# Optimization experiments

Measured on AMD Instinct MI355X. Metric: run time of the kernel, lower is better.

Reference implementation:

```python
import jax, jax.numpy as jnp
import numpy as np

EPS = 1e-5
DEPTH = 3
NQ = 12


def _bn(x, g, b):
    # BatchNorm1d in training mode: batch statistics, biased variance
    mu = x.mean(0)
    var = x.var(0)
    return (x - mu) / jnp.sqrt(var + EPS) * g + b


def _ln(x, g, b):
    mu = x.mean(-1, keepdims=True)
    var = x.var(-1, keepdims=True)
    return (x - mu) / jnp.sqrt(var + EPS) * g + b


def _apply_1q(s, U, q):
    # s: [B, 2^NQ] complex; U: [2,2] (shared) or [B,2,2] (per-sample); qubit q = q-th MSB
    B = s.shape[0]
    s = s.reshape(B, 2 ** q, 2, -1)
    sub = 'ij,bajc->baic' if U.ndim == 2 else 'bij,bajc->baic'
    return jnp.einsum(sub, U, s).reshape(B, -1)


def _apply_cry(s, theta, c):
    # controlled-Ry(theta): control qubit c, target qubit c+1 (adjacent)
    B = s.shape[0]
    s = s.reshape(B, 2 ** c, 2, 2, -1)
    co = jnp.cos(theta / 2).astype(s.dtype)
    si = jnp.sin(theta / 2).astype(s.dtype)
    s1 = s[:, :, 1]  # control = |1> block
    new1 = jnp.stack([co * s1[:, :, 0] - si * s1[:, :, 1],
                      si * s1[:, :, 0] + co * s1[:, :, 1]], axis=2)
    s = jnp.concatenate([s[:, :, :1], new1[:, :, None]], axis=2)
    return s.reshape(B, -1)


def _measure(s):
    # P(qubit q measures |1>) for each qubit
    p = jnp.abs(s) ** 2  # [B, 2^NQ]
    B = p.shape[0]
    probs = [p.reshape(B, 2 ** q, 2, -1).sum(axis=(1, 3))[:, 1] for q in range(NQ)]
    return jnp.stack(probs, axis=1)  # [B, NQ]


def _rot_mats(rot):
    # fused Rz(rz) @ Ry(ry) @ Rx(rx) for each (depth, qubit) -> [DEPTH, NQ, 2, 2]
    hx, hy, hz = rot[..., 0] / 2, rot[..., 1] / 2, rot[..., 2] / 2
    cx, sx = jnp.cos(hx), jnp.sin(hx)
    Rx = jnp.stack([jnp.stack([cx + 0j, -1j * sx], -1),
                    jnp.stack([-1j * sx, cx + 0j], -1)], -2)
    cy, sy = jnp.cos(hy), jnp.sin(hy)
    Ry = jnp.stack([jnp.stack([cy, -sy], -1),
                    jnp.stack([sy, cy], -1)], -2).astype(jnp.complex64)
    ez = jnp.exp(-1j * hz)
    z0 = jnp.zeros_like(ez)
    Rz = jnp.stack([jnp.stack([ez, z0], -1),
                    jnp.stack([z0, jnp.conj(ez)], -1)], -2)
    return jnp.einsum('...ij,...jk,...kl->...il', Rz, Ry, Rx).astype(jnp.complex64)


def _quantum_layer(x, We, be, gi, bi, rot, ent, Wd, bd, go, bo):
    e = jnp.tanh(_bn(x @ We.T + be, gi, bi))  # [B, NQ]
    nrm = jnp.linalg.norm(e, axis=1, keepdims=True)
    a = jnp.where(nrm > 0, e / nrm, e)        # per-sample L2-normalized amplitudes
    B = x.shape[0]
    s = jnp.zeros((B, 2 ** NQ), jnp.complex64).at[:, 0].set(1.0)
    # amplitude encoding: Ry(2*arcsin(|a|)) then phase pi (sign) if a<0 -> diag(1,-1)@Ry
    ang = 2.0 * jnp.arcsin(jnp.clip(jnp.abs(a), 0.0, 1.0))
    c, si = jnp.cos(ang / 2), jnp.sin(ang / 2)
    sg = jnp.where(a < 0, -1.0, 1.0)
    for q in range(NQ):
        U = jnp.stack([jnp.stack([c[:, q], -si[:, q]], -1),
                       jnp.stack([sg[:, q] * si[:, q], sg[:, q] * c[:, q]], -1)],
                      -2).astype(jnp.complex64)  # [B,2,2]
        s = _apply_1q(s, U, q)
    # parameterized circuit: per-qubit fused Rz.Ry.Rx, then nearest-neighbor CRy chain
    U = _rot_mats(rot)
    for d in range(DEPTH):
        for q in range(NQ):
            s = _apply_1q(s, U[d, q], q)
        for i in range(NQ - 1):
            s = _apply_cry(s, ent[d, i], i)
    m = _measure(s)
    return _bn(m @ Wd.T + bd, go, bo)


def setup_inputs() -> dict:
    key = jax.random.key(0)
    ks = jax.random.split(key, 16)
    B, IN, H1, H2, H3, OUT = 512, 512, 512, 512, 1024, 256

    def lin(k, o, i):
        k1, k2 = jax.random.split(k)
        lim = 1.0 / np.sqrt(i)
        return (jax.random.uniform(k1, (o, i), jnp.float32, -lim, lim),
                jax.random.uniform(k2, (o,), jnp.float32, -lim, lim))

    qWe0, qbe0 = lin(ks[1], NQ, IN)
    qWd0, qbd0 = lin(ks[2], H1, NQ)
    qWe1, qbe1 = lin(ks[3], NQ, H1)
    qWd1, qbd1 = lin(ks[4], H2, NQ)
    W2, b2 = lin(ks[5], H3, H2)
    Wo, bo = lin(ks[6], OUT, H3)
    return {
        'x': jax.random.normal(ks[0], (B, IN), jnp.float32),
        'qWe0': qWe0, 'qbe0': qbe0,
        'qgi0': jnp.ones(NQ), 'qbi0': jnp.zeros(NQ),
        'rot0': 0.1 * jax.random.normal(ks[7], (DEPTH, NQ, 3), jnp.float32),
        'ent0': 0.1 * jax.random.normal(ks[8], (DEPTH, NQ - 1), jnp.float32),
        'qWd0': qWd0, 'qbd0': qbd0,
        'qgo0': jnp.ones(H1), 'qbo0': jnp.zeros(H1),
        'qWe1': qWe1, 'qbe1': qbe1,
        'qgi1': jnp.ones(NQ), 'qbi1': jnp.zeros(NQ),
        'rot1': 0.1 * jax.random.normal(ks[9], (DEPTH, NQ, 3), jnp.float32),
        'ent1': 0.1 * jax.random.normal(ks[10], (DEPTH, NQ - 1), jnp.float32),
        'qWd1': qWd1, 'qbd1': qbd1,
        'qgo1': jnp.ones(H2), 'qbo1': jnp.zeros(H2),
        'W2': W2, 'b2': b2, 'ln2g': jnp.ones(H3), 'ln2b': jnp.zeros(H3),
        'Wo': Wo, 'bo': bo, 'lnog': jnp.ones(OUT), 'lnob': jnp.zeros(OUT),
    }


def reference(x, qWe0, qbe0, qgi0, qbi0, rot0, ent0, qWd0, qbd0, qgo0, qbo0,
              qWe1, qbe1, qgi1, qbi1, rot1, ent1, qWd1, qbd1, qgo1, qbo1,
              W2, b2, ln2g, ln2b, Wo, bo, lnog, lnob):
    h = _quantum_layer(x, qWe0, qbe0, qgi0, qbi0, rot0, ent0, qWd0, qbd0, qgo0, qbo0)
    h = _quantum_layer(h, qWe1, qbe1, qgi1, qbi1, rot1, ent1, qWd1, qbd1, qgo1, qbo1)
    h = jax.nn.relu(_ln(h @ W2.T + b2, ln2g, ln2b))  # classical block (dropout = identity, eval)
    return _ln(h @ Wo.T + bo, lnog, lnob)
```

## Files before the change

### kernel.cpp

```cpp
#include <hip/hip_runtime.h>
#include <math.h>

#define EPS   1e-5f
#define NQ    12
#define DEPTH 3
#define BATCH 512
#define DIM   4096

__device__ inline float2 cmul(float2 a, float2 b) {
    return make_float2(a.x*b.x - a.y*b.y, a.x*b.y + a.y*b.x);
}
__device__ inline float2 cmac2(float2 ua, float2 s, float2 ub, float2 p) {
    return make_float2(ua.x*s.x - ua.y*s.y + ub.x*p.x - ub.y*p.y,
                       ua.x*s.y + ua.y*s.x + ub.x*p.y + ub.y*p.x);
}

__global__ void consts_kernel(const float* __restrict__ rot0, const float* __restrict__ ent0,
                              const float* __restrict__ rot1, const float* __restrict__ ent1,
                              float2* __restrict__ Uc, float2* __restrict__ Cc) {
    int t = threadIdx.x;
    if (t < 72) {
        int layer = t / 36, rem = t % 36, d = rem / 12, q = rem % 12;
        const float* rot = layer ? rot1 : rot0;
        float hx = 0.5f * rot[(d*NQ + q)*3 + 0];
        float hy = 0.5f * rot[(d*NQ + q)*3 + 1];
        float hz = 0.5f * rot[(d*NQ + q)*3 + 2];
        float cx = cosf(hx), sx = sinf(hx);
        float cy = cosf(hy), sy = sinf(hy);
        float2 m00 = make_float2( cy*cx,  sy*sx);
        float2 m01 = make_float2(-sy*cx, -cy*sx);
        float2 m10 = make_float2( sy*cx, -cy*sx);
        float2 m11 = make_float2( cy*cx, -sy*sx);
        float2 ez  = make_float2(cosf(hz), -sinf(hz));
        float2 ezc = make_float2(ez.x, -ez.y);
        float2* U = Uc + t*4;
        U[0] = cmul(ez,  m00);
        U[1] = cmul(ez,  m01);
        U[2] = cmul(ezc, m10);
        U[3] = cmul(ezc, m11);
    } else if (t < 72 + 66) {
        int idx = t - 72, layer = idx / 33, rem = idx % 33;
        const float* ent = layer ? ent1 : ent0;
        float th = 0.5f * ent[rem];
        Cc[idx] = make_float2(cosf(th), sinf(th));
    }
}

__global__ __launch_bounds__(256) void encode_rm_kernel(
        const float* __restrict__ X, const float* __restrict__ We,
        const float* __restrict__ be, float* __restrict__ Yraw) {
    __shared__ float w[NQ][512];
    int tid = threadIdx.x;
    {
        const float4* src = (const float4*)We;
        float4* dst = (float4*)&w[0][0];
        #pragma unroll
        for (int i = tid; i < NQ*512/4; i += 256) dst[i] = src[i];
    }
    __syncthreads();
    int wave = tid >> 6, lane = tid & 63;
    int b = blockIdx.x * 4 + wave;
    const float4* xr = (const float4*)(X + (size_t)b * 512);
    float acc[NQ] = {};
    #pragma unroll
    for (int j = 0; j < 2; ++j) {
        float4 xv = xr[lane + 64*j];
        #pragma unroll
        for (int q = 0; q < NQ; ++q) {
            float4 wv = ((const float4*)&w[q][0])[lane + 64*j];
            acc[q] += xv.x*wv.x + xv.y*wv.y + xv.z*wv.z + xv.w*wv.w;
        }
    }
    #pragma unroll
    for (int q = 0; q < NQ; ++q) {
        float v = acc[q];
        #pragma unroll
        for (int off = 32; off; off >>= 1) v += __shfl_xor(v, off);
        if (lane == q) Yraw[b*NQ + q] = v + be[q];
    }
}

__global__ __launch_bounds__(512) void bn_tanh_kernel(
        const float* __restrict__ Yraw,
        const float* __restrict__ gi, const float* __restrict__ bi,
        float* __restrict__ A) {
    int b = threadIdx.x;
    float v[NQ];
    #pragma unroll
    for (int q = 0; q < NQ; ++q) v[q] = Yraw[b*NQ + q];
    __shared__ float2 red[NQ][8];
    int lane = b & 63, wave = b >> 6;
    #pragma unroll
    for (int q = 0; q < NQ; ++q) {
        float2 t = make_float2(v[q], v[q]*v[q]);
        for (int off = 32; off; off >>= 1) { t.x += __shfl_down(t.x, off); t.y += __shfl_down(t.y, off); }
        if (lane == 0) red[q][wave] = t;
    }
    __syncthreads();
    #pragma unroll
    for (int q = 0; q < NQ; ++q) {
        float s = 0.f, s2 = 0.f;
        #pragma unroll
        for (int wv = 0; wv < 8; ++wv) { s += red[q][wv].x; s2 += red[q][wv].y; }
        float mu  = s  * (1.f/512.f);
        float var = s2 * (1.f/512.f) - mu*mu;
        A[b*NQ + q] = tanhf((v[q] - mu) * rsqrtf(var + EPS) * gi[q] + bi[q]);
    }
}

__device__ inline int swz(int a) { return a ^ ((a >> 4) & 15); }

template<int L> __device__ inline int ampl(int tid, int k) {
    if constexpr (L == 1) return (k << 8) | tid;
    else if constexpr (L == 2) return ((tid & 0xE0) << 4) | (k << 5) | (tid & 0x1F);
    else if constexpr (L == 3) return ((tid & 0xFC) << 4) | (k << 2) | (tid & 3);
    else return (tid << 4) | k;
}

template<int F, int T>
__device__ inline void remap(float2* amp, float2* lds2, int tid) {
    #pragma unroll
    for (int k = 0; k < 16; ++k) lds2[swz(ampl<F>(tid, k))] = amp[k];
    __syncthreads();
    #pragma unroll
    for (int k = 0; k < 16; ++k) amp[k] = lds2[swz(ampl<T>(tid, k))];
    __syncthreads();
}

template<int BP>
__device__ inline void one_q(float2* amp, float2 u00, float2 u01, float2 u10, float2 u11) {
    #pragma unroll
    for (int g = 0; g < 8; ++g) {
        const int j0 = ((g >> BP) << (BP+1)) | (g & ((1<<BP)-1));
        const int j1 = j0 | (1 << BP);
        float2 a0 = amp[j0], a1 = amp[j1];
        amp[j0] = cmac2(u00, a0, u01, a1);
        amp[j1] = cmac2(u10, a0, u11, a1);
    }
}

template<int CB, int TB>
__device__ inline void cry_rr(float2* amp, float co, float si) {
    #pragma unroll
    for (int m = 0; m < 16; ++m) {
        if (((m >> CB) & 1) && !((m >> TB) & 1)) {
            const int j1 = m | (1 << TB);
            float2 a0 = amp[m], a1 = amp[j1];
            amp[m]  = make_float2(co*a0.x - si*a1.x, co*a0.y - si*a1.y);
            amp[j1] = make_float2(si*a0.x + co*a1.x, si*a0.y + co*a1.y);
        }
    }
}

__global__ __launch_bounds__(256) void qsim_kernel(
        const float* __restrict__ A, const float2* __restrict__ UcAll,
        const float2* __restrict__ CcAll, int layer, float* __restrict__ mout) {
    int b = blockIdx.x, tid = threadIdx.x;
    const float2* Uc = UcAll + layer * DEPTH * NQ * 4;
    const float2* Cc = CcAll + layer * DEPTH * (NQ - 1);
    __shared__ float2 lds2[DIM];
    __shared__ float red[NQ][4];

    float av[NQ]; float n2 = 0.f;
    #pragma unroll
    for (int q = 0; q < NQ; ++q) { av[q] = A[b*NQ + q]; n2 += av[q]*av[q]; }
    float scn = (n2 > 0.f) ? rsqrtf(n2) : 1.f;
    float2 v0[NQ], v1[NQ];
    #pragma unroll
    for (int q = 0; q < NQ; ++q) {
        float a  = av[q] * scn;
        float sv = fminf(fabsf(a), 1.f);
        float c  = sqrtf(fmaxf(1.f - sv*sv, 0.f));
        float ss = (a < 0.f) ? -sv : sv;
        const float2* U = Uc + q*4;
        v0[q] = make_float2(U[0].x*c + U[1].x*ss, U[0].y*c + U[1].y*ss);
        v1[q] = make_float2(U[2].x*c + U[3].x*ss, U[2].y*c + U[3].y*ss);
    }
    float2 common = make_float2(1.f, 0.f);
    #pragma unroll
    for (int bb = 0; bb < 8; ++bb)
        common = cmul(common, ((tid >> bb) & 1) ? v1[11-bb] : v0[11-bb]);
    float2 amp[16];
    amp[0] = common;
    #pragma unroll
    for (int m = 0; m < 4; ++m) {
        const int q = 3 - m;
        #pragma unroll
        for (int k = 0; k < (1<<m); ++k) {
            amp[k | (1<<m)] = cmul(amp[k], v1[q]);
            amp[k]          = cmul(amp[k], v0[q]);
        }
    }

    for (int d = 0; d < DEPTH; ++d) {
        const float2* Ud = Uc + d*NQ*4;
        const float2* Cd = Cc + d*(NQ-1);
        if (d > 0) {
            remap<4,1>(amp, lds2, tid);
            one_q<3>(amp, Ud[0],  Ud[1],  Ud[2],  Ud[3]);
            one_q<2>(amp, Ud[4],  Ud[5],  Ud[6],  Ud[7]);
            one_q<1>(amp, Ud[8],  Ud[9],  Ud[10], Ud[11]);
            one_q<0>(amp, Ud[12], Ud[13], Ud[14], Ud[15]);
        }
        cry_rr<3,2>(amp, Cd[0].x, Cd[0].y);
        cry_rr<2,1>(amp, Cd[1].x, Cd[1].y);
        cry_rr<1,0>(amp, Cd[2].x, Cd[2].y);
        remap<1,2>(amp, lds2, tid);
        if (d > 0) {
            one_q<2>(amp, Ud[16], Ud[17], Ud[18], Ud[19]);
            one_q<1>(amp, Ud[20], Ud[21], Ud[22], Ud[23]);
            one_q<0>(amp, Ud[24], Ud[25], Ud[26], Ud[27]);
        }
        cry_rr<3,2>(amp, Cd[3].x, Cd[3].y);
        cry_rr<2,1>(amp, Cd[4].x, Cd[4].y);
        cry_rr<1,0>(amp, Cd[5].x, Cd[5].y);
        remap<2,3>(amp, lds2, tid);
        if (d > 0) {
            one_q<2>(amp, Ud[28], Ud[29], Ud[30], Ud[31]);
            one_q<1>(amp, Ud[32], Ud[33], Ud[34], Ud[35]);
            one_q<0>(amp, Ud[36], Ud[37], Ud[38], Ud[39]);
        }
        cry_rr<3,2>(amp, Cd[6].x, Cd[6].y);
        cry_rr<2,1>(amp, Cd[7].x, Cd[7].y);
        cry_rr<1,0>(amp, Cd[8].x, Cd[8].y);
        remap<3,4>(amp, lds2, tid);
        if (d > 0) {
            one_q<1>(amp, Ud[40], Ud[41], Ud[42], Ud[43]);
            one_q<0>(amp, Ud[44], Ud[45], Ud[46], Ud[47]);
        }
        cry_rr<2,1>(amp, Cd[9].x,  Cd[9].y);
        cry_rr<1,0>(amp, Cd[10].x, Cd[10].y);
    }

    float msum = 0.f, p8 = 0.f, p9 = 0.f, p10 = 0.f, p11 = 0.f;
    #pragma unroll
    for (int k = 0; k < 16; ++k) {
        float m = amp[k].x*amp[k].x + amp[k].y*amp[k].y;
        msum += m;
        if (k & 8) p8  += m;
        if (k & 4) p9  += m;
        if (k & 2) p10 += m;
        if (k & 1) p11 += m;
    }
    int lane = tid & 63, wave = tid >> 6;
    #pragma unroll
    for (int q = 0; q < NQ; ++q) {
        float v;
        if (q < 8)        v = ((tid >> (7-q)) & 1) ? msum : 0.f;
        else if (q == 8)  v = p8;
        else if (q == 9)  v = p9;
        else if (q == 10) v = p10;
        else              v = p11;
        #pragma unroll
        for (int off = 32; off; off >>= 1) v += __shfl_xor(v, off);
        if (lane == 0) red[q][wave] = v;
    }
    __syncthreads();
    if (tid < NQ)
        mout[b*NQ + tid] = red[tid][0] + red[tid][1] + red[tid][2] + red[tid][3];
}

__global__ __launch_bounds__(512) void decode_kernel(
        const float* __restrict__ m, const float* __restrict__ Wd,
        const float* __restrict__ bd, const float* __restrict__ go,
        const float* __restrict__ bo, float* __restrict__ outT) {
    int h = blockIdx.x, b = threadIdx.x;
    __shared__ float sm[BATCH * 13];
    __shared__ float2 red[8];
    for (int idx = b; idx < BATCH * NQ; idx += 512) {
        int bb = idx / NQ, q = idx - bb * NQ;
        sm[bb*13 + q] = m[idx];
    }
    __syncthreads();
    float z = bd[h];
    #pragma unroll
    for (int q = 0; q < NQ; ++q) z += sm[b*13 + q] * Wd[h*NQ + q];

    float2 v = make_float2(z, z*z);
    int lane = b & 63, wave = b >> 6;
    for (int off = 32; off; off >>= 1) { v.x += __shfl_down(v.x, off); v.y += __shfl_down(v.y, off); }
    if (lane == 0) red[wave] = v;
    __syncthreads();
    float s = 0.f, s2 = 0.f;
    #pragma unroll
    for (int wv = 0; wv < 8; ++wv) { s += red[wv].x; s2 += red[wv].y; }
    float mu  = s  * (1.f/512.f);
    float var = s2 * (1.f/512.f) - mu*mu;
    outT[(size_t)h*BATCH + b] = (z - mu) * rsqrtf(var + EPS) * go[h] + bo[h];
}

__global__ __launch_bounds__(256) void transpose512_kernel(
        const float* __restrict__ in, float* __restrict__ out) {
    __shared__ float t[64][68];
    int tx = blockIdx.x & 7, ty = blockIdx.x >> 3;
    int tid = threadIdx.x;
    int c4 = (tid & 15) * 4, rr = tid >> 4;
    #pragma unroll
    for (int i = 0; i < 4; ++i) {
        int h = ty*64 + rr + i*16;
        float4 v = *(const float4*)(in + (size_t)h*512 + tx*64 + c4);
        t[c4+0][rr+i*16] = v.x; t[c4+1][rr+i*16] = v.y;
        t[c4+2][rr+i*16] = v.z; t[c4+3][rr+i*16] = v.w;
    }
    __syncthreads();
    #pragma unroll
    for (int i = 0; i < 4; ++i) {
        int bb = tx*64 + rr + i*16;
        float4 o = *(const float4*)&t[rr+i*16][c4];
        *(float4*)(out + (size_t)bb*512 + ty*64 + c4) = o;
    }
}

__global__ __launch_bounds__(256) void gemm1_kernel(
        const float* __restrict__ AT,
        const float* __restrict__ W,
        float* __restrict__ Cpart) {
    __shared__ float As[2][32][64];
    __shared__ float Bs[2][32][68];
    const int b0 = blockIdx.x * 64, j0 = blockIdx.y * 64;
    const int kbase = blockIdx.z * 256;
    float* C = Cpart + (size_t)blockIdx.z * 512 * 1024;
    const int tid = threadIdx.x;
    const int tr = tid >> 4, tc = tid & 15;
    const int a_kk = tid >> 4, a_f4 = tid & 15;
    const int b_jj = tid >> 3, b_k4 = (tid & 7) * 4;
    float4 ra0, ra1, rb0, rb1;
    float acc[4][4] = {};

    {
        const int k0 = kbase;
        ra0 = *(const float4*)(AT + (size_t)(k0 + a_kk)*512 + b0 + a_f4*4);
        ra1 = *(const float4*)(AT + (size_t)(k0 + a_kk + 16)*512 + b0 + a_f4*4);
        rb0 = *(const float4*)(W + (size_t)(j0 + b_jj)*512 + k0 + b_k4);
        rb1 = *(const float4*)(W + (size_t)(j0 + b_jj + 32)*512 + k0 + b_k4);
        *(float4*)&As[0][a_kk][a_f4*4] = ra0;
        *(float4*)&As[0][a_kk+16][a_f4*4] = ra1;
        Bs[0][b_k4+0][b_jj] = rb0.x; Bs[0][b_k4+1][b_jj] = rb0.y;
        Bs[0][b_k4+2][b_jj] = rb0.z; Bs[0][b_k4+3][b_jj] = rb0.w;
        Bs[0][b_k4+0][b_jj+32] = rb1.x; Bs[0][b_k4+1][b_jj+32] = rb1.y;
        Bs[0][b_k4+2][b_jj+32] = rb1.z; Bs[0][b_k4+3][b_jj+32] = rb1.w;
    }
    __syncthreads();
    for (int s = 0; s < 8; ++s) {
        if (s < 7) {
            const int k0 = kbase + (s+1)*32;
            ra0 = *(const float4*)(AT + (size_t)(k0 + a_kk)*512 + b0 + a_f4*4);
            ra1 = *(const float4*)(AT + (size_t)(k0 + a_kk + 16)*512 + b0 + a_f4*4);
            rb0 = *(const float4*)(W + (size_t)(j0 + b_jj)*512 + k0 + b_k4);
            rb1 = *(const float4*)(W + (size_t)(j0 + b_jj + 32)*512 + k0 + b_k4);
        }
        const int bf = s & 1;
        #pragma unroll
        for (int kk = 0; kk < 32; ++kk) {
            float4 a  = *(const float4*)&As[bf][kk][tr*4];
            float4 bv = *(const float4*)&Bs[bf][kk][tc*4];
            acc[0][0] += a.x*bv.x; acc[0][1] += a.x*bv.y; acc[0][2] += a.x*bv.z; acc[0][3] += a.x*bv.w;
            acc[1][0] += a.y*bv.x; acc[1][1] += a.y*bv.y; acc[1][2] += a.y*bv.z; acc[1][3] += a.y*bv.w;
            acc[2][0] += a.z*bv.x; acc[2][1] += a.z*bv.y; acc[2][2] += a.z*bv.z; acc[2][3] += a.z*bv.w;
            acc[3][0] += a.w*bv.x; acc[3][1] += a.w*bv.y; acc[3][2] += a.w*bv.z; acc[3][3] += a.w*bv.w;
        }
        if (s < 7) {
            const int nb = bf ^ 1;
            *(float4*)&As[nb][a_kk][a_f4*4] = ra0;
            *(float4*)&As[nb][a_kk+16][a_f4*4] = ra1;
            Bs[nb][b_k4+0][b_jj] = rb0.x; Bs[nb][b_k4+1][b_jj] = rb0.y;
            Bs[nb][b_k4+2][b_jj] = rb0.z; Bs[nb][b_k4+3][b_jj] = rb0.w;
            Bs[nb][b_k4+0][b_jj+32] = rb1.x; Bs[nb][b_k4+1][b_jj+32] = rb1.y;
            Bs[nb][b_k4+2][b_jj+32] = rb1.z; Bs[nb][b_k4+3][b_jj+32] = rb1.w;
        }
        __syncthreads();
    }
    #pragma unroll
    for (int r = 0; r < 4; ++r) {
        float4 o = make_float4(acc[r][0], acc[r][1], acc[r][2], acc[r][3]);
        *(float4*)(C + (size_t)(b0 + tr*4 + r)*1024 + j0 + tc*4) = o;
    }
}

__global__ __launch_bounds__(256) void gemm2_kernel(
        const float* __restrict__ Amat,
        const float* __restrict__ W,
        float* __restrict__ Cpart) {
    __shared__ float As[2][32][68];
    __shared__ float Bs[2][32][68];
    const int b0 = blockIdx.x * 64, j0 = blockIdx.y * 64;
    const int kbase = blockIdx.z * 128;
    float* C = Cpart + (size_t)blockIdx.z * 512 * 256;
    const int tid = threadIdx.x;
    const int tr = tid >> 4, tc = tid & 15;
    const int l_r = tid >> 3, l_k4 = (tid & 7) * 4;
    float4 ra0, ra1, rb0, rb1;
    float acc[4][4] = {};

    {
        const int k0 = kbase;
        ra0 = *(const float4*)(Amat + (size_t)(b0 + l_r)*1024 + k0 + l_k4);
        ra1 = *(const float4*)(Amat + (size_t)(b0 + l_r + 32)*1024 + k0 + l_k4);
        rb0 = *(const float4*)(W + (size_t)(j0 + l_r)*1024 + k0 + l_k4);
        rb1 = *(const float4*)(W + (size_t)(j0 + l_r + 32)*1024 + k0 + l_k4);
        As[0][l_k4+0][l_r] = ra0.x; As[0][l_k4+1][l_r] = ra0.y;
        As[0][l_k4+2][l_r] = ra0.z; As[0][l_k4+3][l_r] = ra0.w;
        As[0][l_k4+0][l_r+32] = ra1.x; As[0][l_k4+1][l_r+32] = ra1.y;
        As[0][l_k4+2][l_r+32] = ra1.z; As[0][l_k4+3][l_r+32] = ra1.w;
        Bs[0][l_k4+0][l_r] = rb0.x; Bs[0][l_k4+1][l_r] = rb0.y;
        Bs[0][l_k4+2][l_r] = rb0.z; Bs[0][l_k4+3][l_r] = rb0.w;
        Bs[0][l_k4+0][l_r+32] = rb1.x; Bs[0][l_k4+1][l_r+32] = rb1.y;
        Bs[0][l_k4+2][l_r+32] = rb1.z; Bs[0][l_k4+3][l_r+32] = rb1.w;
    }
    __syncthreads();
    for (int s = 0; s < 4; ++s) {
        if (s < 3) {
            const int k0 = kbase + (s+1)*32;
            ra0 = *(const float4*)(Amat + (size_t)(b0 + l_r)*1024 + k0 + l_k4);
            ra1 = *(const float4*)(Amat + (size_t)(b0 + l_r + 32)*1024 + k0 + l_k4);
            rb0 = *(const float4*)(W + (size_t)(j0 + l_r)*1024 + k0 + l_k4);
            rb1 = *(const float4*)(W + (size_t)(j0 + l_r + 32)*1024 + k0 + l_k4);
        }
        const int bf = s & 1;
        #pragma unroll
        for (int kk = 0; kk < 32; ++kk) {
            float4 a  = *(const float4*)&As[bf][kk][tr*4];
            float4 bv = *(const float4*)&Bs[bf][kk][tc*4];
            acc[0][0] += a.x*bv.x; acc[0][1] += a.x*bv.y; acc[0][2] += a.x*bv.z; acc[0][3] += a.x*bv.w;
            acc[1][0] += a.y*bv.x; acc[1][1] += a.y*bv.y; acc[1][2] += a.y*bv.z; acc[1][3] += a.y*bv.w;
            acc[2][0] += a.z*bv.x; acc[2][1] += a.z*bv.y; acc[2][2] += a.z*bv.z; acc[2][3] += a.z*bv.w;
            acc[3][0] += a.w*bv.x; acc[3][1] += a.w*bv.y; acc[3][2] += a.w*bv.z; acc[3][3] += a.w*bv.w;
        }
        if (s < 3) {
            const int nb = bf ^ 1;
            As[nb][l_k4+0][l_r] = ra0.x; As[nb][l_k4+1][l_r] = ra0.y;
            As[nb][l_k4+2][l_r] = ra0.z; As[nb][l_k4+3][l_r] = ra0.w;
            As[nb][l_k4+0][l_r+32] = ra1.x; As[nb][l_k4+1][l_r+32] = ra1.y;
            As[nb][l_k4+2][l_r+32] = ra1.z; As[nb][l_k4+3][l_r+32] = ra1.w;
            Bs[nb][l_k4+0][l_r] = rb0.x; Bs[nb][l_k4+1][l_r] = rb0.y;
            Bs[nb][l_k4+2][l_r] = rb0.z; Bs[nb][l_k4+3][l_r] = rb0.w;
            Bs[nb][l_k4+0][l_r+32] = rb1.x; Bs[nb][l_k4+1][l_r+32] = rb1.y;
            Bs[nb][l_k4+2][l_r+32] = rb1.z; Bs[nb][l_k4+3][l_r+32] = rb1.w;
        }
        __syncthreads();
    }
    #pragma unroll
    for (int r = 0; r < 4; ++r) {
        float4 o = make_float4(acc[r][0], acc[r][1], acc[r][2], acc[r][3]);
        *(float4*)(C + (size_t)(b0 + tr*4 + r)*256 + j0 + tc*4) = o;
    }
}

__global__ __launch_bounds__(256) void ln_relu_kernel(
        const float* __restrict__ P,
        const float* __restrict__ bias,
        const float* __restrict__ g, const float* __restrict__ be,
        float* __restrict__ Y) {
    int b = blockIdx.x, tid = threadIdx.x;
    __shared__ float2 red[4];
    const float* p0 = P + (size_t)b * 1024;
    const float* p1 = P + 524288 + (size_t)b * 1024;
    float v0 = p0[tid]     + p1[tid]     + bias[tid];
    float v1 = p0[tid+256] + p1[tid+256] + bias[tid+256];
    float v2 = p0[tid+512] + p1[tid+512] + bias[tid+512];
    float v3 = p0[tid+768] + p1[tid+768] + bias[tid+768];
    float2 v = make_float2(v0+v1+v2+v3, v0*v0+v1*v1+v2*v2+v3*v3);
    int lane = tid & 63, wave = tid >> 6;
    for (int off = 32; off; off >>= 1) { v.x += __shfl_down(v.x, off); v.y += __shfl_down(v.y, off); }
    if (lane == 0) red[wave] = v;
    __syncthreads();
    float s = 0.f, s2 = 0.f;
    #pragma unroll
    for (int wv = 0; wv < 4; ++wv) { s += red[wv].x; s2 += red[wv].y; }
    float mu  = s  * (1.f/1024.f);
    float var = s2 * (1.f/1024.f) - mu*mu;
    float inv = rsqrtf(var + EPS);
    float* yr = Y + (size_t)b * 1024;
    yr[tid]     = fmaxf((v0-mu)*inv*g[tid]     + be[tid],     0.f);
    yr[tid+256] = fmaxf((v1-mu)*inv*g[tid+256] + be[tid+256], 0.f);
    yr[tid+512] = fmaxf((v2-mu)*inv*g[tid+512] + be[tid+512], 0.f);
    yr[tid+768] = fmaxf((v3-mu)*inv*g[tid+768] + be[tid+768], 0.f);
}

__global__ __launch_bounds__(256) void ln_out_kernel(
        const float* __restrict__ P,
        const float* __restrict__ bias,
        const float* __restrict__ g, const float* __restrict__ be,
        float* __restrict__ Y) {
    int b = blockIdx.x, tid = threadIdx.x;
    __shared__ float2 red[4];
    float v0 = bias[tid];
    #pragma unroll
    for (int z = 0; z < 8; ++z) v0 += P[(size_t)z*131072 + (size_t)b*256 + tid];
    float2 v = make_float2(v0, v0*v0);
    int lane = tid & 63, wave = tid >> 6;
    for (int off = 32; off; off >>= 1) { v.x += __shfl_down(v.x, off); v.y += __shfl_down(v.y, off); }
    if (lane == 0) red[wave] = v;
    __syncthreads();
    float s = 0.f, s2 = 0.f;
    #pragma unroll
    for (int wv = 0; wv < 4; ++wv) { s += red[wv].x; s2 += red[wv].y; }
    float mu  = s  * (1.f/256.f);
    float var = s2 * (1.f/256.f) - mu*mu;
    Y[(size_t)b*256 + tid] = (v0 - mu) * rsqrtf(var + EPS) * g[tid] + be[tid];
}

extern "C" void kernel_launch(void* const* d_in, const int* in_sizes, int n_in,
                              void* d_out, int out_size, void* d_ws, size_t ws_size,
                              hipStream_t stream) {
    const float* x    = (const float*)d_in[0];
    const float* qWe0 = (const float*)d_in[1];
    const float* qbe0 = (const float*)d_in[2];
    const float* qgi0 = (const float*)d_in[3];
    const float* qbi0 = (const float*)d_in[4];
    const float* rot0 = (const float*)d_in[5];
    const float* ent0 = (const float*)d_in[6];
    const float* qWd0 = (const float*)d_in[7];
    const float* qbd0 = (const float*)d_in[8];
    const float* qgo0 = (const float*)d_in[9];
    const float* qbo0 = (const float*)d_in[10];
    const float* qWe1 = (const float*)d_in[11];
    const float* qbe1 = (const float*)d_in[12];
    const float* qgi1 = (const float*)d_in[13];
    const float* qbi1 = (const float*)d_in[14];
    const float* rot1 = (const float*)d_in[15];
    const float* ent1 = (const float*)d_in[16];
    const float* qWd1 = (const float*)d_in[17];
    const float* qbd1 = (const float*)d_in[18];
    const float* qgo1 = (const float*)d_in[19];
    const float* qbo1 = (const float*)d_in[20];
    const float* W2   = (const float*)d_in[21];
    const float* b2   = (const float*)d_in[22];
    const float* ln2g = (const float*)d_in[23];
    const float* ln2b = (const float*)d_in[24];
    const float* Wo   = (const float*)d_in[25];
    const float* bo   = (const float*)d_in[26];
    const float* lnog = (const float*)d_in[27];
    const float* lnob = (const float*)d_in[28];
    float* out = (float*)d_out;
    float* ws  = (float*)d_ws;

    float2* Uc = (float2*)ws;
    float2* Cc = Uc + 288;
    float* A0   = ws + 1024;
    float* m0   = ws + 7168;
    float* A1   = ws + 13312;
    float* m1   = ws + 19456;
    float* Yraw = ws + 25600;
    float* h1T  = ws + 32768;
    float* h1   = ws + 294912;
    float* h2T  = ws + 32768;
    float* t3p  = ws + 557056;
    float* t3n  = ws + 1605632;
    float* t4p  = ws + 557056;

    hipLaunchKernelGGL(consts_kernel, dim3(1), dim3(256), 0, stream,
                       rot0, ent0, rot1, ent1, Uc, Cc);

    hipLaunchKernelGGL(encode_rm_kernel, dim3(128), dim3(256), 0, stream,
                       x, qWe0, qbe0, Yraw);
    hipLaunchKernelGGL(bn_tanh_kernel, dim3(1), dim3(512), 0, stream,
                       Yraw, qgi0, qbi0, A0);
    hipLaunchKernelGGL(qsim_kernel, dim3(512), dim3(256), 0, stream,
                       A0, Uc, Cc, 0, m0);
    hipLaunchKernelGGL(decode_kernel, dim3(512), dim3(512), 0, stream,
                       m0, qWd0, qbd0, qgo0, qbo0, h1T);
    hipLaunchKernelGGL(transpose512_kernel, dim3(64), dim3(256), 0, stream,
                       h1T, h1);

    hipLaunchKernelGGL(encode_rm_kernel, dim3(128), dim3(256), 0, stream,
                       h1, qWe1, qbe1, Yraw);
    hipLaunchKernelGGL(bn_tanh_kernel, dim3(1), dim3(512), 0, stream,
                       Yraw, qgi1, qbi1, A1);
    hipLaunchKernelGGL(qsim_kernel, dim3(512), dim3(256), 0, stream,
                       A1, Uc, Cc, 1, m1);
    hipLaunchKernelGGL(decode_kernel, dim3(512), dim3(512), 0, stream,
                       m1, qWd1, qbd1, qgo1, qbo1, h2T);

    hipLaunchKernelGGL(gemm1_kernel, dim3(8, 16, 2), dim3(256), 0, stream,
                       h2T, W2, t3p);
    hipLaunchKernelGGL(ln_relu_kernel, dim3(512), dim3(256), 0, stream,
                       t3p, b2, ln2g, ln2b, t3n);
    hipLaunchKernelGGL(gemm2_kernel, dim3(8, 4, 8), dim3(256), 0, stream,
                       t3n, Wo, t4p);
    hipLaunchKernelGGL(ln_out_kernel, dim3(512), dim3(256), 0, stream,
                       t4p, bo, lnog, lnob, out);
}
```

Measured before the change: 235.1 us.

## Fuse BN-tanh into qsim, merge consts into encode, drop transpose, retile GEMMs

Folds the single-block batch-norm/tanh kernel into each qsim block: every block recomputes the column statistics from Yraw, which removes a serial one-block launch. The constants computation moves into an extra block of the first encode kernel. The second encode reads the transposed decode output directly, so the transpose kernel is gone. The GEMMs get smaller tiles and more split-K or grid blocks, and the workspace is re-laid out. In exchange there are redundant per-block reductions, plus zeroing of Yraw1 inside qsim, which suggests encode1 accumulates with atomics.

```diff
diff --git a/kernel.cpp b/kernel.cpp
--- a/kernel.cpp
+++ b/kernel.cpp
@@ -15,10 +15,150 @@
                        ua.x*s.y + ua.y*s.x + ub.x*p.y + ub.y*p.x);
 }
 
-__global__ void consts_kernel(const float* __restrict__ rot0, const float* __restrict__ ent0,
-                              const float* __restrict__ rot1, const float* __restrict__ ent1,
-                              float2* __restrict__ Uc, float2* __restrict__ Cc) {
-    int t = threadIdx.x;
+__device__ inline int swz(int a) { return a ^ ((a >> 4) & 15); }
+
+template<int L> __device__ inline int ampl(int tid, int k) {
+    if constexpr (L == 1) return (k << 8) | tid;
+    else if constexpr (L == 2) return ((tid & 0xE0) << 4) | (k << 5) | (tid & 0x1F);
+    else if constexpr (L == 3) return ((tid & 0xFC) << 4) | (k << 2) | (tid & 3);
+    else return (tid << 4) | k;
+}
+
+template<int F, int T>
+__device__ inline void remap(float2* amp, float2* lds2, int tid) {
+    #pragma unroll
+    for (int k = 0; k < 16; ++k) lds2[swz(ampl<F>(tid, k))] = amp[k];
+    __syncthreads();
+    #pragma unroll
+    for (int k = 0; k < 16; ++k) amp[k] = lds2[swz(ampl<T>(tid, k))];
+    __syncthreads();
+}
+
+template<int BP>
+__device__ inline void one_q(float2* amp, float2 u00, float2 u01, float2 u10, float2 u11) {
+    #pragma unroll
+    for (int g = 0; g < 8; ++g) {
+        const int j0 = ((g >> BP) << (BP+1)) | (g & ((1<<BP)-1));
+        const int j1 = j0 | (1 << BP);
+        float2 a0 = amp[j0], a1 = amp[j1];
+        amp[j0] = cmac2(u00, a0, u01, a1);
+        amp[j1] = cmac2(u10, a0, u11, a1);
+    }
+}
+
+template<int CB, int TB>
+__device__ inline void cry_rr(float2* amp, float co, float si) {
+    #pragma unroll
+    for (int m = 0; m < 16; ++m) {
+        if (((m >> CB) & 1) && !((m >> TB) & 1)) {
+            const int j1 = m | (1 << TB);
+            float2 a0 = amp[m], a1 = amp[j1];
+            amp[m]  = make_float2(co*a0.x - si*a1.x, co*a0.y - si*a1.y);
+            amp[j1] = make_float2(si*a0.x + co*a1.x, si*a0.y + co*a1.y);
+        }
+    }
+}
+
+__device__ void qsim_core(float2* amp, float2* lds2, float* redm,
+                          const float2* Uc, const float2* Cc,
+                          int tid, int b, float* mout) {
+    for (int d = 0; d < DEPTH; ++d) {
+        const float2* Ud = Uc + d*NQ*4;
+        const float2* Cd = Cc + d*(NQ-1);
+        if (d > 0) {
+            remap<4,1>(amp, lds2, tid);
+            one_q<3>(amp, Ud[0],  Ud[1],  Ud[2],  Ud[3]);
+            one_q<2>(amp, Ud[4],  Ud[5],  Ud[6],  Ud[7]);
+            one_q<1>(amp, Ud[8],  Ud[9],  Ud[10], Ud[11]);
+            one_q<0>(amp, Ud[12], Ud[13], Ud[14], Ud[15]);
+        }
+        cry_rr<3,2>(amp, Cd[0].x, Cd[0].y);
+        cry_rr<2,1>(amp, Cd[1].x, Cd[1].y);
+        cry_rr<1,0>(amp, Cd[2].x, Cd[2].y);
+        remap<1,2>(amp, lds2, tid);
+        if (d > 0) {
+            one_q<2>(amp, Ud[16], Ud[17], Ud[18], Ud[19]);
+            one_q<1>(amp, Ud[20], Ud[21], Ud[22], Ud[23]);
+            one_q<0>(amp, Ud[24], Ud[25], Ud[26], Ud[27]);
+        }
+        cry_rr<3,2>(amp, Cd[3].x, Cd[3].y);
+        cry_rr<2,1>(amp, Cd[4].x, Cd[4].y);
+        cry_rr<1,0>(amp, Cd[5].x, Cd[5].y);
+        remap<2,3>(amp, lds2, tid);
+        if (d > 0) {
+            one_q<2>(amp, Ud[28], Ud[29], Ud[30], Ud[31]);
+            one_q<1>(amp, Ud[32], Ud[33], Ud[34], Ud[35]);
+            one_q<0>(amp, Ud[36], Ud[37], Ud[38], Ud[39]);
+        }
+        cry_rr<3,2>(amp, Cd[6].x, Cd[6].y);
+        cry_rr<2,1>(amp, Cd[7].x, Cd[7].y);
+        cry_rr<1,0>(amp, Cd[8].x, Cd[8].y);
+        remap<3,4>(amp, lds2, tid);
+        if (d > 0) {
+            one_q<1>(amp, Ud[40], Ud[41], Ud[42], Ud[43]);
+            one_q<0>(amp, Ud[44], Ud[45], Ud[46], Ud[47]);
+        }
+        cry_rr<2,1>(amp, Cd[9].x,  Cd[9].y);
+        cry_rr<1,0>(amp, Cd[10].x, Cd[10].y);
+    }
+    float msum = 0.f, p8 = 0.f, p9 = 0.f, p10 = 0.f, p11 = 0.f;
+    #pragma unroll
+    for (int k = 0; k < 16; ++k) {
+        float m = amp[k].x*amp[k].x + amp[k].y*amp[k].y;
+        msum += m;
+        if (k & 8) p8  += m;
+        if (k & 4) p9  += m;
+        if (k & 2) p10 += m;
+        if (k & 1) p11 += m;
+    }
+    int lane = tid & 63, wave = tid >> 6;
+    #pragma unroll
+    for (int q = 0; q < NQ; ++q) {
+        float v;
+        if (q < 8)        v = ((tid >> (7-q)) & 1) ? msum : 0.f;
+        else if (q == 8)  v = p8;
+        else if (q == 9)  v = p9;
+        else if (q == 10) v = p10;
+        else              v = p11;
+        #pragma unroll
+        for (int off = 32; off; off >>= 1) v += __shfl_xor(v, off);
+        if (lane == 0) redm[q*4 + wave] = v;
+    }
+    __syncthreads();
+    if (tid < NQ)
+        mout[b*NQ + tid] = redm[tid*4] + redm[tid*4+1] + redm[tid*4+2] + redm[tid*4+3];
+}
+
+__device__ void qsim_init(float2* amp, const float* a, const float2* Uc, int tid) {
+    float2 v0[NQ], v1[NQ];
+    #pragma unroll
+    for (int q = 0; q < NQ; ++q) {
+        float sv = fminf(fabsf(a[q]), 1.f);
+        float c  = sqrtf(fmaxf(1.f - sv*sv, 0.f));
+        float ss = (a[q] < 0.f) ? -sv : sv;
+        const float2* U = Uc + q*4;
+        v0[q] = make_float2(U[0].x*c + U[1].x*ss, U[0].y*c + U[1].y*ss);
+        v1[q] = make_float2(U[2].x*c + U[3].x*ss, U[2].y*c + U[3].y*ss);
+    }
+    float2 common = make_float2(1.f, 0.f);
+    #pragma unroll
+    for (int bb = 0; bb < 8; ++bb)
+        common = cmul(common, ((tid >> bb) & 1) ? v1[11-bb] : v0[11-bb]);
+    amp[0] = common;
+    #pragma unroll
+    for (int m = 0; m < 4; ++m) {
+        const int q = 3 - m;
+        #pragma unroll
+        for (int k = 0; k < (1<<m); ++k) {
+            amp[k | (1<<m)] = cmul(amp[k], v1[q]);
+            amp[k]          = cmul(amp[k], v0[q]);
+        }
+    }
+}
+
+__device__ void consts_body(int t,
+        const float* rot0, const float* ent0, const float* rot1, const float* ent1,
+        float2* Uc, float2* Cc) {
     if (t < 72) {
         int layer = t / 36, rem = t % 36, d = rem / 12, q = rem % 12;
         const float* rot = layer ? rot1 : rot0;
@@ -46,16 +186,23 @@
     }
 }
 
-__global__ __launch_bounds__(256) void encode_rm_kernel(
+__global__ __launch_bounds__(256) void encode0_consts_kernel(
         const float* __restrict__ X, const float* __restrict__ We,
-        const float* __restrict__ be, float* __restrict__ Yraw) {
+        const float* __restrict__ be, float* __restrict__ Yraw,
+        const float* __restrict__ rot0, const float* __restrict__ ent0,
+        const float* __restrict__ rot1, const float* __restrict__ ent1,
+        float2* __restrict__ Uc, float2* __restrict__ Cc) {
+    int tid = threadIdx.x;
+    if (blockIdx.x == 128) {
+        consts_body(tid, rot0, ent0, rot1, ent1, Uc, Cc);
+        return;
+    }
     __shared__ float w[NQ][512];
-    int tid = threadIdx.x;
     {
         const float4* src = (const float4*)We;
         float4* dst = (float4*)&w[0][0];
         #pragma unroll
-        for (int i = tid; i < NQ*512/4; i += 256) dst[i] = src[i];
+        for (int i = tid; i < NQ*128; i += 256) dst[i] = src[i];
     }
     __syncthreads();
     int wave = tid >> 6, lane = tid & 63;
@@ -80,184 +227,64 @@
     }
 }
 
-__global__ __launch_bounds__(512) void bn_tanh_kernel(
-        const float* __restrict__ Yraw,
-        const float* __restrict__ gi, const float* __restrict__ bi,
-        float* __restrict__ A) {
-    int b = threadIdx.x;
-    float v[NQ];
-    #pragma unroll
-    for (int q = 0; q < NQ; ++q) v[q] = Yraw[b*NQ + q];
-    __shared__ float2 red[NQ][8];
-    int lane = b & 63, wave = b >> 6;
+__global__ __launch_bounds__(256) void qsim_fused_kernel(
+        const float* __restrict__ Yraw, const float* __restrict__ gi,
+        const float* __restrict__ bi, const float2* __restrict__ UcAll,
+        const float2* __restrict__ CcAll, int layer,
+        float* __restrict__ mout, float* __restrict__ zeroY) {
+    int blk = blockIdx.x, tid = threadIdx.x;
+    const float2* UcL = UcAll + layer * DEPTH * NQ * 4;
+    const float2* CcL = CcAll + layer * DEPTH * (NQ - 1);
+    __shared__ float2 lds2[DIM];
+    __shared__ float sred[96];
+    if (zeroY && tid < NQ) zeroY[blk*NQ + tid] = 0.f;
+    float sum[NQ] = {}, sq[NQ] = {};
+    const float4* Y4 = (const float4*)Yraw;
+    #pragma unroll
+    for (int j = 0; j < 6; ++j) {
+        float4 v = Y4[tid*6 + j];
+        int q0 = (j*4) % 12;
+        sum[q0+0]+=v.x; sq[q0+0]+=v.x*v.x;
+        sum[q0+1]+=v.y; sq[q0+1]+=v.y*v.y;
+        sum[q0+2]+=v.z; sq[q0+2]+=v.z*v.z;
+        sum[q0+3]+=v.w; sq[q0+3]+=v.w*v.w;
+    }
+    int lane = tid & 63, wave = tid >> 6;
     #pragma unroll
     for (int q = 0; q < NQ; ++q) {
-        float2 t = make_float2(v[q], v[q]*v[q]);
-        for (int off = 32; off; off >>= 1) { t.x += __shfl_down(t.x, off); t.y += __shfl_down(t.y, off); }
-        if (lane == 0) red[q][wave] = t;
-    }
-    __syncthreads();
+        #pragma unroll
+        for (int off = 32; off; off >>= 1) {
+            sum[q] += __shfl_xor(sum[q], off);
+            sq[q]  += __shfl_xor(sq[q],  off);
+        }
+    }
+    if (lane == 0) {
+        #pragma unroll
+        for (int q = 0; q < NQ; ++q) {
+            sred[wave*24 + q]      = sum[q];
+            sred[wave*24 + 12 + q] = sq[q];
+        }
+    }
+    __syncthreads();
+    float a[NQ]; float n2 = 0.f;
+    const float* yr = Yraw + blk*NQ;
     #pragma unroll
     for (int q = 0; q < NQ; ++q) {
-        float s = 0.f, s2 = 0.f;
-        #pragma unroll
-        for (int wv = 0; wv < 8; ++wv) { s += red[q][wv].x; s2 += red[q][wv].y; }
+        float s  = sred[q]    + sred[24+q] + sred[48+q] + sred[72+q];
+        float s2 = sred[12+q] + sred[36+q] + sred[60+q] + sred[84+q];
         float mu  = s  * (1.f/512.f);
         float var = s2 * (1.f/512.f) - mu*mu;
-        A[b*NQ + q] = tanhf((v[q] - mu) * rsqrtf(var + EPS) * gi[q] + bi[q]);
-    }
-}
-
-__device__ inline int swz(int a) { return a ^ ((a >> 4) & 15); }
-
-template<int L> __device__ inline int ampl(int tid, int k) {
-    if constexpr (L == 1) return (k << 8) | tid;
-    else if constexpr (L == 2) return ((tid & 0xE0) << 4) | (k << 5) | (tid & 0x1F);
-    else if constexpr (L == 3) return ((tid & 0xFC) << 4) | (k << 2) | (tid & 3);
-    else return (tid << 4) | k;
-}
-
-template<int F, int T>
-__device__ inline void remap(float2* amp, float2* lds2, int tid) {
-    #pragma unroll
-    for (int k = 0; k < 16; ++k) lds2[swz(ampl<F>(tid, k))] = amp[k];
-    __syncthreads();
-    #pragma unroll
-    for (int k = 0; k < 16; ++k) amp[k] = lds2[swz(ampl<T>(tid, k))];
-    __syncthreads();
-}
-
-template<int BP>
-__device__ inline void one_q(float2* amp, float2 u00, float2 u01, float2 u10, float2 u11) {
-    #pragma unroll
-    for (int g = 0; g < 8; ++g) {
-        const int j0 = ((g >> BP) << (BP+1)) | (g & ((1<<BP)-1));
-        const int j1 = j0 | (1 << BP);
-        float2 a0 = amp[j0], a1 = amp[j1];
-        amp[j0] = cmac2(u00, a0, u01, a1);
-        amp[j1] = cmac2(u10, a0, u11, a1);
-    }
-}
-
-template<int CB, int TB>
-__device__ inline void cry_rr(float2* amp, float co, float si) {
-    #pragma unroll
-    for (int m = 0; m < 16; ++m) {
-        if (((m >> CB) & 1) && !((m >> TB) & 1)) {
-            const int j1 = m | (1 << TB);
-            float2 a0 = amp[m], a1 = amp[j1];
-            amp[m]  = make_float2(co*a0.x - si*a1.x, co*a0.y - si*a1.y);
-            amp[j1] = make_float2(si*a0.x + co*a1.x, si*a0.y + co*a1.y);
-        }
-    }
-}
-
-__global__ __launch_bounds__(256) void qsim_kernel(
-        const float* __restrict__ A, const float2* __restrict__ UcAll,
-        const float2* __restrict__ CcAll, int layer, float* __restrict__ mout) {
-    int b = blockIdx.x, tid = threadIdx.x;
-    const float2* Uc = UcAll + layer * DEPTH * NQ * 4;
-    const float2* Cc = CcAll + layer * DEPTH * (NQ - 1);
-    __shared__ float2 lds2[DIM];
-    __shared__ float red[NQ][4];
-
-    float av[NQ]; float n2 = 0.f;
-    #pragma unroll
-    for (int q = 0; q < NQ; ++q) { av[q] = A[b*NQ + q]; n2 += av[q]*av[q]; }
+        float val = (yr[q] - mu) * rsqrtf(var + EPS) * gi[q] + bi[q];
+        a[q] = tanhf(val);
+        n2 += a[q]*a[q];
+    }
     float scn = (n2 > 0.f) ? rsqrtf(n2) : 1.f;
-    float2 v0[NQ], v1[NQ];
-    #pragma unroll
-    for (int q = 0; q < NQ; ++q) {
-        float a  = av[q] * scn;
-        float sv = fminf(fabsf(a), 1.f);
-        float c  = sqrtf(fmaxf(1.f - sv*sv, 0.f));
-        float ss = (a < 0.f) ? -sv : sv;
-        const float2* U = Uc + q*4;
-        v0[q] = make_float2(U[0].x*c + U[1].x*ss, U[0].y*c + U[1].y*ss);
-        v1[q] = make_float2(U[2].x*c + U[3].x*ss, U[2].y*c + U[3].y*ss);
-    }
-    float2 common = make_float2(1.f, 0.f);
-    #pragma unroll
-    for (int bb = 0; bb < 8; ++bb)
-        common = cmul(common, ((tid >> bb) & 1) ? v1[11-bb] : v0[11-bb]);
+    #pragma unroll
+    for (int q = 0; q < NQ; ++q) a[q] *= scn;
+    __syncthreads();
     float2 amp[16];
-    amp[0] = common;
-    #pragma unroll
-    for (int m = 0; m < 4; ++m) {
-        const int q = 3 - m;
-        #pragma unroll
-        for (int k = 0; k < (1<<m); ++k) {
-            amp[k | (1<<m)] = cmul(amp[k], v1[q]);
-            amp[k]          = cmul(amp[k], v0[q]);
-        }
-    }
-
-    for (int d = 0; d < DEPTH; ++d) {
-        const float2* Ud = Uc + d*NQ*4;
-        const float2* Cd = Cc + d*(NQ-1);
-        if (d > 0) {
-            remap<4,1>(amp, lds2, tid);
-            one_q<3>(amp, Ud[0],  Ud[1],  Ud[2],  Ud[3]);
-            one_q<2>(amp, Ud[4],  Ud[5],  Ud[6],  Ud[7]);
-            one_q<1>(amp, Ud[8],  Ud[9],  Ud[10], Ud[11]);
-            one_q<0>(amp, Ud[12], Ud[13], Ud[14], Ud[15]);
-        }
-        cry_rr<3,2>(amp, Cd[0].x, Cd[0].y);
-        cry_rr<2,1>(amp, Cd[1].x, Cd[1].y);
-        cry_rr<1,0>(amp, Cd[2].x, Cd[2].y);
-        remap<1,2>(amp, lds2, tid);
-        if (d > 0) {
-            one_q<2>(amp, Ud[16], Ud[17], Ud[18], Ud[19]);
-            one_q<1>(amp, Ud[20], Ud[21], Ud[22], Ud[23]);
-            one_q<0>(amp, Ud[24], Ud[25], Ud[26], Ud[27]);
-        }
-        cry_rr<3,2>(amp, Cd[3].x, Cd[3].y);
-        cry_rr<2,1>(amp, Cd[4].x, Cd[4].y);
-        cry_rr<1,0>(amp, Cd[5].x, Cd[5].y);
-        remap<2,3>(amp, lds2, tid);
-        if (d > 0) {
-            one_q<2>(amp, Ud[28], Ud[29], Ud[30], Ud[31]);
-            one_q<1>(amp, Ud[32], Ud[33], Ud[34], Ud[35]);
-            one_q<0>(amp, Ud[36], Ud[37], Ud[38], Ud[39]);
-        }
-        cry_rr<3,2>(amp, Cd[6].x, Cd[6].y);
-        cry_rr<2,1>(amp, Cd[7].x, Cd[7].y);
-        cry_rr<1,0>(amp, Cd[8].x, Cd[8].y);
-        remap<3,4>(amp, lds2, tid);
-        if (d > 0) {
-            one_q<1>(amp, Ud[40], Ud[41], Ud[42], Ud[43]);
-            one_q<0>(amp, Ud[44], Ud[45], Ud[46], Ud[47]);
-        }
-        cry_rr<2,1>(amp, Cd[9].x,  Cd[9].y);
-        cry_rr<1,0>(amp, Cd[10].x, Cd[10].y);
-    }
-
-    float msum = 0.f, p8 = 0.f, p9 = 0.f, p10 = 0.f, p11 = 0.f;
-    #pragma unroll
-    for (int k = 0; k < 16; ++k) {
-        float m = amp[k].x*amp[k].x + amp[k].y*amp[k].y;
-        msum += m;
-        if (k & 8) p8  += m;
-        if (k & 4) p9  += m;
-        if (k & 2) p10 += m;
-        if (k & 1) p11 += m;
-    }
-    int lane = tid & 63, wave = tid >> 6;
-    #pragma unroll
-    for (int q = 0; q < NQ; ++q) {
-        float v;
-        if (q < 8)        v = ((tid >> (7-q)) & 1) ? msum : 0.f;
-        else if (q == 8)  v = p8;
-        else if (q == 9)  v = p9;
-        else if (q == 10) v = p10;
-        else              v = p11;
-        #pragma unroll
-        for (int off = 32; off; off >>= 1) v += __shfl_xor(v, off);
-        if (lane == 0) red[q][wave] = v;
-    }
-    __syncthreads();
-    if (tid < NQ)
-        mout[b*NQ + tid] = red[tid][0] + red[tid][1] + red[tid][2] + red[tid][3];
+    qsim_init(amp, a, UcL, tid);
+    qsim_core(amp, lds2, sred, UcL, CcL, tid, blk, mout);
 }
 
 __global__ __launch_bounds__(512) void decode_kernel(
@@ -267,15 +294,17 @@
     int h = blockIdx.x, b = threadIdx.x;
     __shared__ float sm[BATCH * 13];
     __shared__ float2 red[8];
-    for (int idx = b; idx < BATCH * NQ; idx += 512) {
-        int bb = idx / NQ, q = idx - bb * NQ;
-        sm[bb*13 + q] = m[idx];
+    const float4* m4 = (const float4*)m;
+    for (int f4 = b; f4 < 1536; f4 += 512) {
+        float4 v = m4[f4];
+        int base = f4*4; int row = base/12; int q = base - row*12;
+        float* dst = sm + row*13 + q;
+        dst[0]=v.x; dst[1]=v.y; dst[2]=v.z; dst[3]=v.w;
     }
     __syncthreads();
     float z = bd[h];
     #pragma unroll
     for (int q = 0; q < NQ; ++q) z += sm[b*13 + q] * Wd[h*NQ + q];
-
     float2 v = make_float2(z, z*z);
     int lane = b & 63, wave = b >> 6;
     for (int off = 32; off; off >>= 1) { v.x += __shfl_down(v.x, off); v.y += __shfl_down(v.y, off); }
@@ -289,36 +318,48 @@
     outT[(size_t)h*BATCH + b] = (z - mu) * rsqrtf(var + EPS) * go[h] + bo[h];
 }
 
-__global__ __launch_bounds__(256) void transpose512_kernel(
-        const float* __restrict__ in, float* __restrict__ out) {
-    __shared__ float t[64][68];
-    int tx = blockIdx.x & 7, ty = blockIdx.x >> 3;
-    int tid = threadIdx.x;
-    int c4 = (tid & 15) * 4, rr = tid >> 4;
-    #pragma unroll
-    for (int i = 0; i < 4; ++i) {
-        int h = ty*64 + rr + i*16;
-        float4 v = *(const float4*)(in + (size_t)h*512 + tx*64 + c4);
-        t[c4+0][rr+i*16] = v.x; t[c4+1][rr+i*16] = v.y;
-        t[c4+2][rr+i*16] = v.z; t[c4+3][rr+i*16] = v.w;
-    }
-    __syncthreads();
-    #pragma unroll
-    for (int i = 0; i < 4; ++i) {
-        int bb = tx*64 + rr + i*16;
-        float4 o = *(const float4*)&t[rr+i*16][c4];
-        *(float4*)(out + (size_t)bb*512 + ty*64 + c4) = o;
+__global__ __launch_bounds__(256) void encode1_kernel(
+        const float* __restrict__ h1T, const float* __restrict__ We,
+        const float* __restrict__ be, float* __restrict__ Yraw1) {
+    __shared__ float w[NQ][512];
+    __shared__ float red[4*64*NQ];
+    int tid = threadIdx.x, blk = blockIdx.x;
+    {
+        const float4* src = (const float4*)We;
+        float4* dst = (float4*)&w[0][0];
+        #pragma unroll
+        for (int i = tid; i < NQ*128; i += 256) dst[i] = src[i];
+    }
+    __syncthreads();
+    int kc = blk >> 3, bc = blk & 7;
+    int bl = tid & 63, hg = tid >> 6;
+    int b = bc*64 + bl;
+    float acc[NQ] = {};
+    #pragma unroll
+    for (int i = 0; i < 16; ++i) {
+        int h = kc*64 + hg*16 + i;
+        float xv = h1T[(size_t)h*512 + b];
+        #pragma unroll
+        for (int q = 0; q < NQ; ++q) acc[q] += xv * w[q][h];
+    }
+    #pragma unroll
+    for (int q = 0; q < NQ; ++q) red[(hg*64 + bl)*NQ + q] = acc[q];
+    __syncthreads();
+    for (int i = tid; i < 64*NQ; i += 256) {
+        int bl2 = i / NQ, q = i - bl2*NQ;
+        float v = red[bl2*NQ+q] + red[(64+bl2)*NQ+q] + red[(128+bl2)*NQ+q] + red[(192+bl2)*NQ+q];
+        if (kc == 0) v += be[q];
+        atomicAdd(&Yraw1[(size_t)(bc*64 + bl2)*NQ + q], v);
     }
 }
 
 __global__ __launch_bounds__(256) void gemm1_kernel(
-        const float* __restrict__ AT,
-        const float* __restrict__ W,
+        const float* __restrict__ AT, const float* __restrict__ W,
         float* __restrict__ Cpart) {
     __shared__ float As[2][32][64];
     __shared__ float Bs[2][32][68];
     const int b0 = blockIdx.x * 64, j0 = blockIdx.y * 64;
-    const int kbase = blockIdx.z * 256;
+    const int kbase = blockIdx.z * 128;
     float* C = Cpart + (size_t)blockIdx.z * 512 * 1024;
     const int tid = threadIdx.x;
     const int tr = tid >> 4, tc = tid & 15;
@@ -326,7 +367,6 @@
     const int b_jj = tid >> 3, b_k4 = (tid & 7) * 4;
     float4 ra0, ra1, rb0, rb1;
     float acc[4][4] = {};
-
     {
         const int k0 = kbase;
         ra0 = *(const float4*)(AT + (size_t)(k0 + a_kk)*512 + b0 + a_f4*4);
@@ -341,8 +381,8 @@
         Bs[0][b_k4+2][b_jj+32] = rb1.z; Bs[0][b_k4+3][b_jj+32] = rb1.w;
     }
     __syncthreads();
-    for (int s = 0; s < 8; ++s) {
-        if (s < 7) {
+    for (int s = 0; s < 4; ++s) {
+        if (s < 3) {
             const int k0 = kbase + (s+1)*32;
             ra0 = *(const float4*)(AT + (size_t)(k0 + a_kk)*512 + b0 + a_f4*4);
             ra1 = *(const float4*)(AT + (size_t)(k0 + a_kk + 16)*512 + b0 + a_f4*4);
@@ -359,7 +399,7 @@
             acc[2][0] += a.z*bv.x; acc[2][1] += a.z*bv.y; acc[2][2] += a.z*bv.z; acc[2][3] += a.z*bv.w;
             acc[3][0] += a.w*bv.x; acc[3][1] += a.w*bv.y; acc[3][2] += a.w*bv.z; acc[3][3] += a.w*bv.w;
         }
-        if (s < 7) {
+        if (s < 3) {
             const int nb = bf ^ 1;
             *(float4*)&As[nb][a_kk][a_f4*4] = ra0;
             *(float4*)&As[nb][a_kk+16][a_f4*4] = ra1;
@@ -377,31 +417,61 @@
     }
 }
 
+__global__ __launch_bounds__(256) void ln_relu_kernel(
+        const float* __restrict__ P, const float* __restrict__ bias,
+        const float* __restrict__ g, const float* __restrict__ be,
+        float* __restrict__ Y) {
+    int b = blockIdx.x, tid = threadIdx.x;
+    __shared__ float2 red[4];
+    float v[4];
+    #pragma unroll
+    for (int j = 0; j < 4; ++j) {
+        int col = tid + j*256;
+        float t = bias[col];
+        #pragma unroll
+        for (int z = 0; z < 4; ++z) t += P[(size_t)z*524288 + (size_t)b*1024 + col];
+        v[j] = t;
+    }
+    float2 r = make_float2(v[0]+v[1]+v[2]+v[3],
+                           v[0]*v[0]+v[1]*v[1]+v[2]*v[2]+v[3]*v[3]);
+    int lane = tid & 63, wave = tid >> 6;
+    for (int off = 32; off; off >>= 1) { r.x += __shfl_down(r.x, off); r.y += __shfl_down(r.y, off); }
+    if (lane == 0) red[wave] = r;
+    __syncthreads();
+    float s = red[0].x + red[1].x + red[2].x + red[3].x;
+    float s2 = red[0].y + red[1].y + red[2].y + red[3].y;
+    float mu  = s  * (1.f/1024.f);
+    float var = s2 * (1.f/1024.f) - mu*mu;
+    float inv = rsqrtf(var + EPS);
+    float* yr = Y + (size_t)b * 1024;
+    #pragma unroll
+    for (int j = 0; j < 4; ++j) {
+        int col = tid + j*256;
+        yr[col] = fmaxf((v[j]-mu)*inv*g[col] + be[col], 0.f);
+    }
+}
+
 __global__ __launch_bounds__(256) void gemm2_kernel(
-        const float* __restrict__ Amat,
-        const float* __restrict__ W,
+        const float* __restrict__ Amat, const float* __restrict__ W,
         float* __restrict__ Cpart) {
-    __shared__ float As[2][32][68];
-    __shared__ float Bs[2][32][68];
-    const int b0 = blockIdx.x * 64, j0 = blockIdx.y * 64;
+    __shared__ __align__(16) char smem[27000];
+    float (*As)[32][36] = (float(*)[32][36])smem;
+    float (*Bs)[32][68] = (float(*)[32][68])(smem + 9216);
+    const int b0 = blockIdx.x * 32, j0 = blockIdx.y * 64;
     const int kbase = blockIdx.z * 128;
     float* C = Cpart + (size_t)blockIdx.z * 512 * 256;
     const int tid = threadIdx.x;
     const int tr = tid >> 4, tc = tid & 15;
     const int l_r = tid >> 3, l_k4 = (tid & 7) * 4;
-    float4 ra0, ra1, rb0, rb1;
-    float acc[4][4] = {};
-
+    float4 ra0, rb0, rb1;
+    float acc[2][4] = {};
     {
         const int k0 = kbase;
         ra0 = *(const float4*)(Amat + (size_t)(b0 + l_r)*1024 + k0 + l_k4);
-        ra1 = *(const float4*)(Amat + (size_t)(b0 + l_r + 32)*1024 + k0 + l_k4);
         rb0 = *(const float4*)(W + (size_t)(j0 + l_r)*1024 + k0 + l_k4);
         rb1 = *(const float4*)(W + (size_t)(j0 + l_r + 32)*1024 + k0 + l_k4);
         As[0][l_k4+0][l_r] = ra0.x; As[0][l_k4+1][l_r] = ra0.y;
         As[0][l_k4+2][l_r] = ra0.z; As[0][l_k4+3][l_r] = ra0.w;
-        As[0][l_k4+0][l_r+32] = ra1.x; As[0][l_k4+1][l_r+32] = ra1.y;
-        As[0][l_k4+2][l_r+32] = ra1.z; As[0][l_k4+3][l_r+32] = ra1.w;
         Bs[0][l_k4+0][l_r] = rb0.x; Bs[0][l_k4+1][l_r] = rb0.y;
         Bs[0][l_k4+2][l_r] = rb0.z; Bs[0][l_k4+3][l_r] = rb0.w;
         Bs[0][l_k4+0][l_r+32] = rb1.x; Bs[0][l_k4+1][l_r+32] = rb1.y;
@@ -412,26 +482,21 @@
         if (s < 3) {
             const int k0 = kbase + (s+1)*32;
             ra0 = *(const float4*)(Amat + (size_t)(b0 + l_r)*1024 + k0 + l_k4);
-            ra1 = *(const float4*)(Amat + (size_t)(b0 + l_r + 32)*1024 + k0 + l_k4);
             rb0 = *(const float4*)(W + (size_t)(j0 + l_r)*1024 + k0 + l_k4);
             rb1 = *(const float4*)(W + (size_t)(j0 + l_r + 32)*1024 + k0 + l_k4);
         }
         const int bf = s & 1;
         #pragma unroll
         for (int kk = 0; kk < 32; ++kk) {
-            float4 a  = *(const float4*)&As[bf][kk][tr*4];
+            float a0 = As[bf][kk][tr*2], a1 = As[bf][kk][tr*2+1];
             float4 bv = *(const float4*)&Bs[bf][kk][tc*4];
-            acc[0][0] += a.x*bv.x; acc[0][1] += a.x*bv.y; acc[0][2] += a.x*bv.z; acc[0][3] += a.x*bv.w;
-            acc[1][0] += a.y*bv.x; acc[1][1] += a.y*bv.y; acc[1][2] += a.y*bv.z; acc[1][3] += a.y*bv.w;
-            acc[2][0] += a.z*bv.x; acc[2][1] += a.z*bv.y; acc[2][2] += a.z*bv.z; acc[2][3] += a.z*bv.w;
-            acc[3][0] += a.w*bv.x; acc[3][1] += a.w*bv.y; acc[3][2] += a.w*bv.z; acc[3][3] += a.w*bv.w;
+            acc[0][0] += a0*bv.x; acc[0][1] += a0*bv.y; acc[0][2] += a0*bv.z; acc[0][3] += a0*bv.w;
+            acc[1][0] += a1*bv.x; acc[1][1] += a1*bv.y; acc[1][2] += a1*bv.z; acc[1][3] += a1*bv.w;
         }
         if (s < 3) {
             const int nb = bf ^ 1;
             As[nb][l_k4+0][l_r] = ra0.x; As[nb][l_k4+1][l_r] = ra0.y;
             As[nb][l_k4+2][l_r] = ra0.z; As[nb][l_k4+3][l_r] = ra0.w;
-            As[nb][l_k4+0][l_r+32] = ra1.x; As[nb][l_k4+1][l_r+32] = ra1.y;
-            As[nb][l_k4+2][l_r+32] = ra1.z; As[nb][l_k4+3][l_r+32] = ra1.w;
             Bs[nb][l_k4+0][l_r] = rb0.x; Bs[nb][l_k4+1][l_r] = rb0.y;
             Bs[nb][l_k4+2][l_r] = rb0.z; Bs[nb][l_k4+3][l_r] = rb0.w;
             Bs[nb][l_k4+0][l_r+32] = rb1.x; Bs[nb][l_k4+1][l_r+32] = rb1.y;
@@ -440,46 +505,14 @@
         __syncthreads();
     }
     #pragma unroll
-    for (int r = 0; r < 4; ++r) {
+    for (int r = 0; r < 2; ++r) {
         float4 o = make_float4(acc[r][0], acc[r][1], acc[r][2], acc[r][3]);
-        *(float4*)(C + (size_t)(b0 + tr*4 + r)*256 + j0 + tc*4) = o;
-    }
-}
-
-__global__ __launch_bounds__(256) void ln_relu_kernel(
-        const float* __restrict__ P,
-        const float* __restrict__ bias,
-        const float* __restrict__ g, const float* __restrict__ be,
-        float* __restrict__ Y) {
-    int b = blockIdx.x, tid = threadIdx.x;
-    __shared__ float2 red[4];
-    const float* p0 = P + (size_t)b * 1024;
-    const float* p1 = P + 524288 + (size_t)b * 1024;
-    float v0 = p0[tid]     + p1[tid]     + bias[tid];
-    float v1 = p0[tid+256] + p1[tid+256] + bias[tid+256];
-    float v2 = p0[tid+512] + p1[tid+512] + bias[tid+512];
-    float v3 = p0[tid+768] + p1[tid+768] + bias[tid+768];
-    float2 v = make_float2(v0+v1+v2+v3, v0*v0+v1*v1+v2*v2+v3*v3);
-    int lane = tid & 63, wave = tid >> 6;
-    for (int off = 32; off; off >>= 1) { v.x += __shfl_down(v.x, off); v.y += __shfl_down(v.y, off); }
-    if (lane == 0) red[wave] = v;
-    __syncthreads();
-    float s = 0.f, s2 = 0.f;
-    #pragma unroll
-    for (int wv = 0; wv < 4; ++wv) { s += red[wv].x; s2 += red[wv].y; }
-    float mu  = s  * (1.f/1024.f);
-    float var = s2 * (1.f/1024.f) - mu*mu;
-    float inv = rsqrtf(var + EPS);
-    float* yr = Y + (size_t)b * 1024;
-    yr[tid]     = fmaxf((v0-mu)*inv*g[tid]     + be[tid],     0.f);
-    yr[tid+256] = fmaxf((v1-mu)*inv*g[tid+256] + be[tid+256], 0.f);
-    yr[tid+512] = fmaxf((v2-mu)*inv*g[tid+512] + be[tid+512], 0.f);
-    yr[tid+768] = fmaxf((v3-mu)*inv*g[tid+768] + be[tid+768], 0.f);
+        *(float4*)(C + (size_t)(b0 + tr*2 + r)*256 + j0 + tc*4) = o;
+    }
 }
 
 __global__ __launch_bounds__(256) void ln_out_kernel(
-        const float* __restrict__ P,
-        const float* __restrict__ bias,
+        const float* __restrict__ P, const float* __restrict__ bias,
         const float* __restrict__ g, const float* __restrict__ be,
         float* __restrict__ Y) {
     int b = blockIdx.x, tid = threadIdx.x;
@@ -492,9 +525,8 @@
     for (int off = 32; off; off >>= 1) { v.x += __shfl_down(v.x, off); v.y += __shfl_down(v.y, off); }
     if (lane == 0) red[wave] = v;
     __syncthreads();
-    float s = 0.f, s2 = 0.f;
-    #pragma unroll
-    for (int wv = 0; wv < 4; ++wv) { s += red[wv].x; s2 += red[wv].y; }
+    float s = red[0].x + red[1].x + red[2].x + red[3].x;
+    float s2 = red[0].y + red[1].y + red[2].y + red[3].y;
     float mu  = s  * (1.f/256.f);
     float var = s2 * (1.f/256.f) - mu*mu;
     Y[(size_t)b*256 + tid] = (v0 - mu) * rsqrtf(var + EPS) * g[tid] + be[tid];
@@ -535,48 +567,35 @@
     float* out = (float*)d_out;
     float* ws  = (float*)d_ws;
 
-    float2* Uc = (float2*)ws;
-    float2* Cc = Uc + 288;
-    float* A0   = ws + 1024;
-    float* m0   = ws + 7168;
-    float* A1   = ws + 13312;
-    float* m1   = ws + 19456;
-    float* Yraw = ws + 25600;
-    float* h1T  = ws + 32768;
-    float* h1   = ws + 294912;
-    float* h2T  = ws + 32768;
-    float* t3p  = ws + 557056;
-    float* t3n  = ws + 1605632;
-    float* t4p  = ws + 557056;
-
-    hipLaunchKernelGGL(consts_kernel, dim3(1), dim3(256), 0, stream,
-                       rot0, ent0, rot1, ent1, Uc, Cc);
-
-    hipLaunchKernelGGL(encode_rm_kernel, dim3(128), dim3(256), 0, stream,
-                       x, qWe0, qbe0, Yraw);
-    hipLaunchKernelGGL(bn_tanh_kernel, dim3(1), dim3(512), 0, stream,
-                       Yraw, qgi0, qbi0, A0);
-    hipLaunchKernelGGL(qsim_kernel, dim3(512), dim3(256), 0, stream,
-                       A0, Uc, Cc, 0, m0);
+    float2* Uc   = (float2*)ws;
+    float2* Cc   = Uc + 288;
+    float* Yraw0 = ws + 1024;
+    float* m0    = ws + 7680;
+    float* Yraw1 = ws + 14336;
+    float* m1    = ws + 20992;
+    float* h1T   = ws + 65536;
+    float* h2T   = ws + 589824;
+    float* t3p   = ws + 851968;
+    float* t3n   = ws + 2949120;
+    float* t4p   = ws + 3473408;
+
+    hipLaunchKernelGGL(encode0_consts_kernel, dim3(129), dim3(256), 0, stream,
+                       x, qWe0, qbe0, Yraw0, rot0, ent0, rot1, ent1, Uc, Cc);
+    hipLaunchKernelGGL(qsim_fused_kernel, dim3(512), dim3(256), 0, stream,
+                       Yraw0, qgi0, qbi0, Uc, Cc, 0, m0, Yraw1);
     hipLaunchKernelGGL(decode_kernel, dim3(512), dim3(512), 0, stream,
                        m0, qWd0, qbd0, qgo0, qbo0, h1T);
-    hipLaunchKernelGGL(transpose512_kernel, dim3(64), dim3(256), 0, stream,
-                       h1T, h1);
-
-    hipLaunchKernelGGL(encode_rm_kernel, dim3(128), dim3(256), 0, stream,
-                       h1, qWe1, qbe1, Yraw);
-    hipLaunchKernelGGL(bn_tanh_kernel, dim3(1), dim3(512), 0, stream,
-                       Yraw, qgi1, qbi1, A1);
-    hipLaunchKernelGGL(qsim_kernel, dim3(512), dim3(256), 0, stream,
-                       A1, Uc, Cc, 1, m1);
+    hipLaunchKernelGGL(encode1_kernel, dim3(64), dim3(256), 0, stream,
+                       h1T, qWe1, qbe1, Yraw1);
+    hipLaunchKernelGGL(qsim_fused_kernel, dim3(512), dim3(256), 0, stream,
+                       Yraw1, qgi1, qbi1, Uc, Cc, 1, m1, (float*)nullptr);
     hipLaunchKernelGGL(decode_kernel, dim3(512), dim3(512), 0, stream,
                        m1, qWd1, qbd1, qgo1, qbo1, h2T);
-
-    hipLaunchKernelGGL(gemm1_kernel, dim3(8, 16, 2), dim3(256), 0, stream,
+    hipLaunchKernelGGL(gemm1_kernel, dim3(8, 16, 4), dim3(256), 0, stream,
                        h2T, W2, t3p);
     hipLaunchKernelGGL(ln_relu_kernel, dim3(512), dim3(256), 0, stream,
                        t3p, b2, ln2g, ln2b, t3n);
-    hipLaunchKernelGGL(gemm2_kernel, dim3(8, 4, 8), dim3(256), 0, stream,
+    hipLaunchKernelGGL(gemm2_kernel, dim3(16, 4, 8), dim3(256), 0, stream,
                        t3n, Wo, t4p);
     hipLaunchKernelGGL(ln_out_kernel, dim3(512), dim3(256), 0, stream,
                        t4p, bo, lnog, lnob, out);
```

Result: faster. 223.2 us (-5.1%).
